# Kernel optimization log

Hardware: AMD Instinct MI355X
Metric: run time of the kernel (lower is better)

The kernel has to match this reference:

```python
import jax, jax.numpy as jnp
from jax import lax
import numpy as np

STRIDES = [4, 8, 16, 32, 64]
SIZES = [32, 64, 128, 256, 512]
RATIOS = [0.5, 1.0, 2.0]
PRE_NMS = 1000   # test-mode pre_nms_topk per level
POST_NMS = 1000  # test-mode post_nms_topk
NMS_THRESH = 0.7
NEG = -1e9
SCALE_CLAMP = float(np.log(1000.0 / 16.0))


def _anchor_bases(size):
    # one size, 3 aspect ratios (h/w); detectron2-style bases centered at 0
    area = float(size) * float(size)
    rows = []
    for ar in RATIOS:
        w = np.sqrt(area / ar)
        h = ar * w
        rows.append([-w / 2.0, -h / 2.0, w / 2.0, h / 2.0])
    return jnp.asarray(np.array(rows, dtype=np.float32))  # [3,4]


def _level_anchors(H, W, stride, bases):
    sx = jnp.arange(W, dtype=jnp.float32) * stride
    sy = jnp.arange(H, dtype=jnp.float32) * stride
    yy, xx = jnp.meshgrid(sy, sx, indexing='ij')
    shifts = jnp.stack([xx, yy, xx, yy], axis=-1).reshape(-1, 1, 4)  # [H*W,1,4]
    return (shifts + bases[None, :, :]).reshape(-1, 4)  # [H*W*3,4]


def _conv(x, w, b, pad):
    y = lax.conv_general_dilated(x, w, (1, 1), [(pad, pad), (pad, pad)],
                                 dimension_numbers=('NCHW', 'OIHW', 'NCHW'))
    return y + b[None, :, None, None]


def _decode(anchors, deltas):
    # anchors [R,4], deltas [B,R,4] -> boxes [B,R,4] (x1,y1,x2,y2)
    w = anchors[:, 2] - anchors[:, 0]
    h = anchors[:, 3] - anchors[:, 1]
    cx = anchors[:, 0] + 0.5 * w
    cy = anchors[:, 1] + 0.5 * h
    dx, dy = deltas[..., 0], deltas[..., 1]
    dw = jnp.minimum(deltas[..., 2], SCALE_CLAMP)
    dh = jnp.minimum(deltas[..., 3], SCALE_CLAMP)
    px = dx * w + cx
    py = dy * h + cy
    pw = jnp.exp(dw) * w
    ph = jnp.exp(dh) * h
    return jnp.stack([px - 0.5 * pw, py - 0.5 * ph, px + 0.5 * pw, py + 0.5 * ph], axis=-1)


def _pairwise_iou(b):
    x1 = jnp.maximum(b[:, None, 0], b[None, :, 0])
    y1 = jnp.maximum(b[:, None, 1], b[None, :, 1])
    x2 = jnp.minimum(b[:, None, 2], b[None, :, 2])
    y2 = jnp.minimum(b[:, None, 3], b[None, :, 3])
    inter = jnp.clip(x2 - x1, 0.0) * jnp.clip(y2 - y1, 0.0)
    area = (b[:, 2] - b[:, 0]) * (b[:, 3] - b[:, 1])
    return inter / (area[:, None] + area[None, :] - inter + 1e-9)


def _nms_single(boxes, scores, valid, lvls, img):
    # greedy batched NMS: level offsets keep levels from suppressing each other
    order = jnp.argsort(-scores)
    b = boxes[order]
    s = scores[order]
    v = valid[order]
    lv = lvls[order].astype(boxes.dtype)
    bo = b + lv[:, None] * (img + 1.0)
    iou = lax.stop_gradient(_pairwise_iou(bo))  # selection is non-differentiable
    T = b.shape[0]
    idxs = jnp.arange(T)

    def step(keep, i):
        supp = (iou[i] > NMS_THRESH) & (idxs > i) & keep[i]
        return keep & ~supp, None

    keep, _ = lax.scan(step, v, jnp.arange(T))
    final = jnp.where(keep, s, NEG)
    topv, topi = lax.top_k(final, POST_NMS)
    return b[topi], topv


def _rpn_forward(feats, w_inter, b_inter, w_logits, b_logits, w_reg, b_reg, image_size):
    img = float(image_size)
    cand_boxes, cand_scores, lvl_ids = [], [], []
    for l, (x, stride, size) in enumerate(zip(feats, STRIDES, SIZES)):
        B, _, H, W = x.shape
        inter = jax.nn.relu(_conv(x, w_inter, b_inter, 1))
        logit = _conv(inter, w_logits, b_logits, 0)        # [B,3,H,W]
        reg = _conv(inter, w_reg, b_reg, 0)                # [B,12,H,W]
        scores = logit.transpose(0, 2, 3, 1).reshape(B, -1)              # [B,H*W*3]
        deltas = reg.reshape(B, 3, 4, H, W).transpose(0, 3, 4, 1, 2).reshape(B, -1, 4)
        anchors = _level_anchors(H, W, stride, _anchor_bases(size))
        boxes = _decode(anchors, deltas)                                  # [B,R,4]
        k = min(PRE_NMS, scores.shape[1])
        topv, topi = lax.top_k(scores, k)
        cand_boxes.append(jnp.take_along_axis(boxes, topi[..., None], axis=1))
        cand_scores.append(topv)
        lvl_ids.append(jnp.full((k,), l, dtype=jnp.int32))
    boxes = jnp.concatenate(cand_boxes, axis=1)   # [B,T,4]
    scores = jnp.concatenate(cand_scores, axis=1) # [B,T]
    lvls = jnp.concatenate(lvl_ids, axis=0)       # [T]
    boxes = jnp.clip(boxes, 0.0, img)
    valid = (boxes[..., 2] > boxes[..., 0]) & (boxes[..., 3] > boxes[..., 1])
    kb, ks = jax.vmap(lambda b, s, v: _nms_single(b, s, v, lvls, img))(boxes, scores, valid)
    return jnp.concatenate([kb, ks[..., None]], axis=-1)  # [B,POST_NMS,5]


def setup_inputs() -> dict:
    key = jax.random.key(0)
    ks = jax.random.split(key, 16)
    C = 256
    inp = {
        'feat_p2': jax.random.normal(ks[0], (2, C, 256, 256), jnp.float32),
        'feat_p3': jax.random.normal(ks[1], (2, C, 128, 128), jnp.float32),
        'feat_p4': jax.random.normal(ks[2], (2, C, 64, 64), jnp.float32),
        'feat_p5': jax.random.normal(ks[3], (2, C, 32, 32), jnp.float32),
        'feat_p6': jax.random.normal(ks[4], (2, C, 16, 16), jnp.float32),
        'w_inter': jax.random.normal(ks[5], (C, C, 3, 3), jnp.float32) * 0.01,
        'b_inter': jnp.zeros((C,), jnp.float32),
        'w_logits': jax.random.normal(ks[6], (3, C, 1, 1), jnp.float32) * 0.01,
        'b_logits': jnp.zeros((3,), jnp.float32),
        'w_reg': jax.random.normal(ks[7], (12, C, 1, 1), jnp.float32) * 0.01,
        'b_reg': jnp.zeros((12,), jnp.float32),
        'image_size': 1024,
    }
    return inp


def reference(feat_p2, feat_p3, feat_p4, feat_p5, feat_p6,
              w_inter, b_inter, w_logits, b_logits, w_reg, b_reg, image_size):
    feats = [feat_p2, feat_p3, feat_p4, feat_p5, feat_p6]
    return _rpn_forward(feats, w_inter, b_inter, w_logits, b_logits, w_reg, b_reg, image_size)
```

## Files before the change

kernel.cpp:

```cpp
#include <hip/hip_runtime.h>
#include <cmath>

typedef unsigned int u32;
typedef unsigned long long u64;

#define TCAND 4768
#define RTOT  261888
#define NW    75
#define NROWS 4800
#define NEGV  -1e9f

__device__ __forceinline__ u32 fkey(float s){
  u32 u = __float_as_uint(s);
  return u ^ ((u >> 31) ? 0xFFFFFFFFu : 0x80000000u);
}

__device__ __forceinline__ void gload_lds16(const float* g, float* l){
  __builtin_amdgcn_global_load_lds((const __attribute__((address_space(1))) void*)g,
                                   (__attribute__((address_space(3))) void*)l, 16, 0, 0);
}
__device__ __forceinline__ void gload_lds4(const float* g, float* l){
  __builtin_amdgcn_global_load_lds((const __attribute__((address_space(1))) void*)g,
                                   (__attribute__((address_space(3))) void*)l, 4, 0, 0);
}

__device__ void bitonic_desc(u64* a, int N, int t, int nt){
  for (int len = 2; len <= N; len <<= 1){
    for (int inc = len >> 1; inc > 0; inc >>= 1){
      __syncthreads();
      for (int idx = t; idx < (N >> 1); idx += nt){
        int i = 2*idx - (idx & (inc - 1));
        int j = i + inc;
        u64 x = a[i], y = a[j];
        bool descR = ((i & len) == 0);
        bool sw = descR ? (x < y) : (x > y);
        if (sw){ a[i] = y; a[j] = x; }
      }
    }
  }
  __syncthreads();
}

__global__ void wtrans(const float* __restrict__ w, float* __restrict__ w_r2,
                       float* __restrict__ zbuf){
  if (blockIdx.x == 0 && threadIdx.x < 16) zbuf[threadIdx.x] = 0.f;
  int idx = blockIdx.x * 256 + threadIdx.x;
  if (idx >= 589824) return;
  int oc = idx / 2304;
  int r  = idx - oc * 2304;
  int ic = r / 9;
  int tap = r - ic * 9;
  w_r2[ic * 2304 + tap * 256 + oc] = w[idx];
}

template<int H, int STRIDEV, int ASIZE, int FOFF>
__device__ __forceinline__ void conv_level(
    int rel, const float* __restrict__ feat, const float* __restrict__ w_r2,
    const float* __restrict__ zbuf,
    const float* __restrict__ b_inter, const float* __restrict__ w_logits,
    const float* __restrict__ b_logits, const float* __restrict__ w_reg,
    const float* __restrict__ b_reg, const int* __restrict__ imgp,
    float* __restrict__ score_base, float* __restrict__ box_base,
    float* lds_w, float* lds_x, float* sbuf)
{
  constexpr int W = H;
  constexpr int TX = H / 8;
  constexpr int TILES = TX * TX;
  const int t = threadIdx.x;
  const int img = rel / TILES;
  const int tile = rel - img * TILES;
  const int x0 = (tile % TX) << 3;
  const int y0 = (tile / TX) << 3;
  const int lane = t & 63;
  const int ocg = lane;
  const int r = t >> 6;
  const int q = r;

  const size_t fb = (size_t)img * 256 * H * W;
  const size_t plane = (size_t)H * W;

  const float* xsrc = zbuf;
  size_t xstep = 0;
  if (q == 1 || q == 2){
    int cell = (q - 1) * 64 + lane;
    int xr = cell / 12, xc = cell - xr * 12;
    int gy = y0 + xr - 1, gx = x0 + xc - 1;
    bool ok = (cell < 120) && (xc < 10) && gy >= 0 && gy < H && gx >= 0 && gx < W;
    if (ok){ xsrc = feat + fb + (size_t)gy * W + gx; xstep = plane; }
  }

  const int c0 = 2 * q, c1 = 2 * q + 1;
  const int cex = (q == 0) ? 16 : ((q == 3) ? 17 : -1);

  float acc[32];
  #pragma unroll
  for (int j = 0; j < 32; j++) acc[j] = 0.f;

  #define STAGE(g_, sb) do { \
    const float* wg_ = w_r2 + (size_t)(g_) * 4608; \
    float* wl_ = lds_w + (sb) * 4608; \
    gload_lds16(wg_ + c0 * 256 + lane * 4, wl_ + c0 * 256); \
    gload_lds16(wg_ + c1 * 256 + lane * 4, wl_ + c1 * 256); \
    if (cex >= 0) gload_lds16(wg_ + cex * 256 + lane * 4, wl_ + cex * 256); \
    if (q == 1 || q == 2){ \
      gload_lds4(xsrc + (size_t)(2 * (g_)) * xstep, \
                 lds_x + (sb) * 256 + (q - 1) * 64); \
      gload_lds4(xsrc + (size_t)(2 * (g_) + 1) * xstep, \
                 lds_x + (sb) * 256 + 128 + (q - 1) * 64); \
    } \
  } while (0)

  STAGE(0, 0);

  int cur = 0;
  #pragma unroll 1
  for (int g = 0; g < 128; ++g){
    __builtin_amdgcn_s_barrier();
    __builtin_amdgcn_sched_barrier(0);
    if (g < 127){
      STAGE(g + 1, cur ^ 1);
    }
    __builtin_amdgcn_sched_barrier(0);
    if (g < 127){
      if (q == 1 || q == 2)      asm volatile("s_waitcnt vmcnt(4)" ::: "memory");
      else if (q == 0 || q == 3) asm volatile("s_waitcnt vmcnt(3)" ::: "memory");
      else                       asm volatile("s_waitcnt vmcnt(2)" ::: "memory");
    } else {
      asm volatile("s_waitcnt vmcnt(0)" ::: "memory");
    }
    __builtin_amdgcn_sched_barrier(0);
    __builtin_amdgcn_s_barrier();
    __builtin_amdgcn_sched_barrier(0);

    __builtin_amdgcn_s_setprio(1);
    const float* wbuf = lds_w + cur * 4608;
    const float* xbuf = lds_x + cur * 256;
    #pragma unroll 1
    for (int icl = 0; icl < 2; icl++){
      const float* wsub = wbuf + icl * 2304;
      const float* xsub = xbuf + icl * 128;
      #pragma unroll
      for (int ky = 0; ky < 3; ky++){
        float xrow[10];
        {
          const float* xp = xsub + (r + ky) * 12;
          *(float4*)&xrow[0] = *(const float4*)xp;
          *(float4*)&xrow[4] = *(const float4*)(xp + 4);
          *(float2*)&xrow[8] = *(const float2*)(xp + 8);
        }
        #pragma unroll
        for (int kx = 0; kx < 3; kx++){
          const int tap = ky * 3 + kx;
          float wk[4];
          *(float4*)&wk[0] = *(const float4*)(wsub + tap * 256 + ocg * 4);
          #pragma unroll
          for (int k = 0; k < 4; k++){
            #pragma unroll
            for (int c = 0; c < 8; c++)
              acc[k * 8 + c] = __builtin_fmaf(wk[k], xrow[c + kx], acc[k * 8 + c]);
          }
        }
      }
    }
    __builtin_amdgcn_s_setprio(0);
    cur ^= 1;
  }
  #undef STAGE

  {
    float bb[4];
    *(float4*)&bb[0] = *(const float4*)(b_inter + ocg * 4);
    #pragma unroll
    for (int k = 0; k < 4; k++)
      #pragma unroll
      for (int c = 0; c < 8; c++)
        acc[k * 8 + c] = fmaxf(acc[k * 8 + c] + bb[k], 0.f);
  }

  const int grp = ocg & 60;
  #pragma unroll 1
  for (int o = 0; o < 15; o++){
    const float* whp = (o < 3) ? (w_logits + o * 256) : (w_reg + (o - 3) * 256);
    float wh4[4];
    *(float4*)&wh4[0] = *(const float4*)(whp + ocg * 4);
    float fin[8];
    #pragma unroll
    for (int c = 0; c < 8; c++){
      float t1 = 0.f;
      #pragma unroll
      for (int k = 0; k < 4; k++) t1 = __builtin_fmaf(wh4[k], acc[k * 8 + c], t1);
      float b1 = __shfl(t1, grp);
      float t2 = b1;
      #pragma unroll
      for (int k = 0; k < 4; k++) t2 = __builtin_fmaf(wh4[k], acc[k * 8 + c], t2);
      float b2 = __shfl(t2, grp + 1);
      float t3 = b2;
      #pragma unroll
      for (int k = 0; k < 4; k++) t3 = __builtin_fmaf(wh4[k], acc[k * 8 + c], t3);
      float b3 = __shfl(t3, grp + 2);
      float t4 = b3;
      #pragma unroll
      for (int k = 0; k < 4; k++) t4 = __builtin_fmaf(wh4[k], acc[k * 8 + c], t4);
      float v = t4 + __shfl_xor(t4, 4);
      v = v + __shfl_xor(v, 8);
      v = v + __shfl_xor(v, 16);
      v = v + __shfl_xor(v, 32);
      fin[c] = v;
    }
    if (ocg == 3){
      #pragma unroll
      for (int c = 0; c < 8; c++) sbuf[(r * 8 + c) * 16 + o] = fin[c];
    }
  }
  __syncthreads();

  if (t < 192){
    int a = t >> 6; int px = t & 63;
    int rr = px >> 3, cc = px & 7;
    int y = y0 + rr, x = x0 + cc;
    float img_f = (float)(*imgp);
    float sc = sbuf[px * 16 + a] + b_logits[a];
    float d0 = sbuf[px * 16 + 3 + a * 4 + 0] + b_reg[a * 4 + 0];
    float d1 = sbuf[px * 16 + 3 + a * 4 + 1] + b_reg[a * 4 + 1];
    float d2 = sbuf[px * 16 + 3 + a * 4 + 2] + b_reg[a * 4 + 2];
    float d3 = sbuf[px * 16 + 3 + a * 4 + 3] + b_reg[a * 4 + 3];
    double ar = (a == 0) ? 0.5 : ((a == 1) ? 1.0 : 2.0);
    double area_d = (double)ASIZE * (double)ASIZE;
    double wd = sqrt(area_d / ar);
    double hd = ar * wd;
    float bx1 = (float)(-wd * 0.5), by1 = (float)(-hd * 0.5);
    float bx2 = (float)( wd * 0.5), by2 = (float)( hd * 0.5);
    float sx = (float)(x * STRIDEV), sy = (float)(y * STRIDEV);
    float ax1 = sx + bx1, ay1 = sy + by1, ax2 = sx + bx2, ay2 = sy + by2;
    float aw = __fsub_rn(ax2, ax1), ah = __fsub_rn(ay2, ay1);
    float acx = __fadd_rn(ax1, __fmul_rn(0.5f, aw));
    float acy = __fadd_rn(ay1, __fmul_rn(0.5f, ah));
    const float CLAMP = (float)4.135166556742356;
    float dwv = fminf(d2, CLAMP), dhv = fminf(d3, CLAMP);
    float pcx = __fadd_rn(__fmul_rn(d0, aw), acx);
    float pcy = __fadd_rn(__fmul_rn(d1, ah), acy);
    float pw = __fmul_rn((float)exp((double)dwv), aw);
    float ph = __fmul_rn((float)exp((double)dhv), ah);
    float hx = __fmul_rn(0.5f, pw), hy = __fmul_rn(0.5f, ph);
    float X1 = __fsub_rn(pcx, hx), Y1 = __fsub_rn(pcy, hy);
    float X2 = __fadd_rn(pcx, hx), Y2 = __fadd_rn(pcy, hy);
    X1 = fminf(fmaxf(X1, 0.f), img_f); Y1 = fminf(fmaxf(Y1, 0.f), img_f);
    X2 = fminf(fmaxf(X2, 0.f), img_f); Y2 = fminf(fmaxf(Y2, 0.f), img_f);
    int gi = (y * W + x) * 3 + a;
    size_t oidx = (size_t)img * RTOT + FOFF + gi;
    score_base[oidx] = sc;
    ((float4*)box_base)[oidx] = make_float4(X1, Y1, X2, Y2);
  }
}

__global__ __launch_bounds__(512, 4) void conv_all(
    const float* __restrict__ f2, const float* __restrict__ f3,
    const float* __restrict__ f4, const float* __restrict__ f5,
    const float* __restrict__ f6, const float* __restrict__ w_r2,
    const float* __restrict__ zbuf,
    const float* __restrict__ b_inter, const float* __restrict__ w_logits,
    const float* __restrict__ b_logits, const float* __restrict__ w_reg,
    const float* __restrict__ b_reg, const int* __restrict__ imgp,
    float* __restrict__ score_base, float* __restrict__ box_base)
{
  __shared__ float lds_w[2 * 4608];
  __shared__ float lds_x[2 * 256];
  float* sbuf = lds_w;
  const int bid = blockIdx.x;
  if (bid < 2048)
    conv_level<256, 4, 32, 0>(bid, f2, w_r2, zbuf, b_inter, w_logits, b_logits, w_reg,
                              b_reg, imgp, score_base, box_base, lds_w, lds_x, sbuf);
  else if (bid < 2560)
    conv_level<128, 8, 64, 196608>(bid - 2048, f3, w_r2, zbuf, b_inter, w_logits, b_logits,
                                   w_reg, b_reg, imgp, score_base, box_base, lds_w, lds_x, sbuf);
  else if (bid < 2688)
    conv_level<64, 16, 128, 245760>(bid - 2560, f4, w_r2, zbuf, b_inter, w_logits, b_logits,
                                    w_reg, b_reg, imgp, score_base, box_base, lds_w, lds_x, sbuf);
  else if (bid < 2720)
    conv_level<32, 32, 256, 258048>(bid - 2688, f5, w_r2, zbuf, b_inter, w_logits, b_logits,
                                    w_reg, b_reg, imgp, score_base, box_base, lds_w, lds_x, sbuf);
  else
    conv_level<16, 64, 512, 261120>(bid - 2720, f6, w_r2, zbuf, b_inter, w_logits, b_logits,
                                    w_reg, b_reg, imgp, score_base, box_base, lds_w, lds_x, sbuf);
}

__global__ __launch_bounds__(1024) void topk_lvl(
    const float* __restrict__ score_base, const float* __restrict__ box_base,
    float* __restrict__ cs, float* __restrict__ cb, int* __restrict__ clvl)
{
  const int lvl = blockIdx.x, b = blockIdx.y;
  const int Rtab[5] = {196608, 49152, 12288, 3072, 768};
  const int Ktab[5] = {1000, 1000, 1000, 1000, 768};
  const int Ftab[5] = {0, 196608, 245760, 258048, 261120};
  const int Ctab[5] = {0, 1000, 2000, 3000, 4000};
  const int R = Rtab[lvl], kk = Ktab[lvl], foff = Ftab[lvl], coff = Ctab[lvl];
  const float* sc = score_base + (size_t)b * RTOT + foff;
  const int t = threadIdx.x;
  const int wv = t >> 6;
  __shared__ u32 histp[16 * 256];
  __shared__ u32 hist[256];
  __shared__ u32 sh_prefix, sh_r;
  __shared__ u32 cgt, ceq;
  __shared__ u64 sel[1024];
  __shared__ u64 eqb[1024];
  if (t == 0){ sh_prefix = 0u; sh_r = (u32)kk; }
  __syncthreads();
  for (int pass = 0; pass < 4; ++pass){
    for (int i = t; i < 4096; i += 1024) histp[i] = 0u;
    __syncthreads();
    u32 prefix = sh_prefix;
    int shift = 24 - 8 * pass;
    u32 maskHi = (pass == 0) ? 0u : (0xFFFFFFFFu << (shift + 8));
    for (int i = t; i < R; i += 1024){
      u32 key = fkey(sc[i]);
      if ((key & maskHi) == prefix) atomicAdd(&histp[wv * 256 + ((key >> shift) & 255u)], 1u);
    }
    __syncthreads();
    if (t < 256){
      u32 s = 0;
      #pragma unroll
      for (int w2 = 0; w2 < 16; w2++) s += histp[w2 * 256 + t];
      hist[t] = s;
    }
    __syncthreads();
    if (t == 0){
      u32 r = sh_r; u32 run = 0; int chosen = 255;
      for (int bv = 255; bv >= 0; --bv){
        u32 c = hist[bv];
        if (run + c >= r){ chosen = bv; break; }
        run += c;
      }
      sh_prefix = prefix | ((u32)chosen << shift);
      sh_r = r - run;
    }
    __syncthreads();
  }
  const u32 Tkey = sh_prefix; const u32 need_eq = sh_r;
  if (t == 0){ cgt = 0u; ceq = 0u; }
  __syncthreads();
  for (int i = t; i < R; i += 1024){
    u32 key = fkey(sc[i]);
    if (key > Tkey){
      u32 p = atomicAdd(&cgt, 1u);
      sel[p] = (((u64)key) << 32) | (u64)(0xFFFFFFFFu - (u32)i);
    } else if (key == Tkey){
      u32 e = atomicAdd(&ceq, 1u);
      if (e < 1024u) eqb[e] = (u64)(0xFFFFFFFFu - (u32)i);
    }
  }
  __syncthreads();
  u32 nGt = cgt; u32 nEq = ceq > 1024u ? 1024u : ceq;
  if ((u32)t >= nEq) eqb[t] = 0ull;
  __syncthreads();
  bitonic_desc(eqb, 1024, t, 1024);
  if ((u32)t < need_eq) sel[nGt + t] = (((u64)Tkey) << 32) | (eqb[t] & 0xFFFFFFFFull);
  if (t >= kk) sel[t] = 0ull;
  __syncthreads();
  bitonic_desc(sel, 1024, t, 1024);
  if (t < kk){
    u64 v = sel[t];
    u32 i = 0xFFFFFFFFu - (u32)(v & 0xFFFFFFFFull);
    int dst = b * TCAND + coff + t;
    cs[dst] = sc[i];
    ((float4*)cb)[dst] = ((const float4*)box_base)[(size_t)b * RTOT + foff + i];
    clvl[dst] = lvl;
  }
}

__global__ __launch_bounds__(1024) void gsort(
    const float* __restrict__ cs, const float* __restrict__ cb, const int* __restrict__ clvl,
    const int* __restrict__ imgp,
    float* __restrict__ s_score, float* __restrict__ s_box, float* __restrict__ obox,
    float* __restrict__ area, int* __restrict__ validarr)
{
  const int b = blockIdx.x, t = threadIdx.x;
  __shared__ u64 arr[8192];
  for (int i = t; i < 8192; i += 1024){
    u64 v = 0ull;
    if (i < TCAND){
      u32 key = fkey(cs[b * TCAND + i]);
      v = (((u64)key) << 32) | (u64)(0xFFFFFFFFu - (u32)i);
    }
    arr[i] = v;
  }
  __syncthreads();
  bitonic_desc(arr, 8192, t, 1024);
  const float img = (float)(*imgp);
  const float off1 = img + 1.0f;
  for (int s = t; s < TCAND; s += 1024){
    u32 ci = 0xFFFFFFFFu - (u32)(arr[s] & 0xFFFFFFFFull);
    int src = b * TCAND + (int)ci;
    int dst = b * TCAND + s;
    float scv = cs[src];
    float4 bx = ((const float4*)cb)[src];
    s_score[dst] = scv;
    ((float4*)s_box)[dst] = bx;
    float lv = (float)clvl[src];
    float tt = __fmul_rn(lv, off1);
    float o0 = __fadd_rn(bx.x, tt), o1 = __fadd_rn(bx.y, tt);
    float o2 = __fadd_rn(bx.z, tt), o3 = __fadd_rn(bx.w, tt);
    ((float4*)obox)[dst] = make_float4(o0, o1, o2, o3);
    area[dst] = __fmul_rn(__fsub_rn(o2, o0), __fsub_rn(o3, o1));
    validarr[dst] = (bx.z > bx.x && bx.w > bx.y) ? 1 : 0;
  }
}

__global__ void iou_mat(const float* __restrict__ obox, const float* __restrict__ area,
                        u64* __restrict__ supp)
{
  const int b = blockIdx.y;
  int wid = blockIdx.x * 256 + threadIdx.x;
  const int total = NW * TCAND;
  if (wid >= total) return;
  int w = wid / TCAND;
  int i = wid - w * TCAND;
  float4 bi = ((const float4*)obox)[b * TCAND + i];
  float ai = area[b * TCAND + i];
  u64 bits = 0ull;
  int jbase = w << 6;
  for (int jj = 0; jj < 64; jj++){
    int j = jbase + jj;
    if (j >= TCAND) break;
    if (j <= i) continue;
    float4 bj = ((const float4*)obox)[b * TCAND + j];
    float xx1 = fmaxf(bi.x, bj.x), yy1 = fmaxf(bi.y, bj.y);
    float xx2 = fminf(bi.z, bj.z), yy2 = fminf(bi.w, bj.w);
    float iw = fmaxf(__fsub_rn(xx2, xx1), 0.f);
    float ih = fmaxf(__fsub_rn(yy2, yy1), 0.f);
    float inter = __fmul_rn(iw, ih);
    float uni = __fadd_rn(__fsub_rn(__fadd_rn(ai, area[b * TCAND + j]), inter), 1e-9f);
    float iou = inter / uni;
    if (iou > 0.7f) bits |= (1ull << jj);
  }
  supp[((size_t)b * NROWS + i) * NW + w] = bits;
}

__global__ __launch_bounds__(64) void nms_scan(const u64* __restrict__ supp,
                                               const int* __restrict__ validarr,
                                               u64* __restrict__ keep_out)
{
  const int b = blockIdx.x;
  const int lane = threadIdx.x;
  u64 rlo = 0ull, rhi = 0ull;
  for (int jj = 0; jj < 64; jj++){
    int i1 = (lane << 6) + jj;
    u64 bad1 = (i1 < TCAND) ? (validarr[b * TCAND + i1] ? 0ull : 1ull) : 1ull;
    rlo |= bad1 << jj;
    int i2 = ((lane + 64) << 6) + jj;
    u64 bad2 = (i2 < TCAND) ? (validarr[b * TCAND + i2] ? 0ull : 1ull) : 1ull;
    rhi |= bad2 << jj;
  }
  for (int c = 0; c < NW; c++){
    u64 rw = (c < 64) ? __shfl(rlo, c) : __shfl(rhi, c - 64);
    u64 diag = supp[((size_t)b * NROWS + (c << 6) + lane) * NW + c];
    for (int s = 0; s < 64; s++){
      if (!((rw >> s) & 1ull)) rw |= __shfl(diag, s);
    }
    if (c < 64){ if (lane == c) rlo = rw; }
    else       { if (lane == c - 64) rhi = rw; }
    u64 kept = ~rw;
    const u64* rowbase = supp + ((size_t)b * NROWS + (c << 6)) * NW;
    u64 rem = kept;
    while (rem){
      int s0 = (int)__builtin_ctzll(rem); rem &= rem - 1;
      int s1 = s0, s2 = s0, s3 = s0;
      if (rem){ s1 = (int)__builtin_ctzll(rem); rem &= rem - 1; }
      if (rem){ s2 = (int)__builtin_ctzll(rem); rem &= rem - 1; }
      if (rem){ s3 = (int)__builtin_ctzll(rem); rem &= rem - 1; }
      u64 a0 = rowbase[(size_t)s0 * NW + lane];
      u64 a1 = rowbase[(size_t)s1 * NW + lane];
      u64 a2 = rowbase[(size_t)s2 * NW + lane];
      u64 a3 = rowbase[(size_t)s3 * NW + lane];
      rlo |= (a0 | a1) | (a2 | a3);
      if (lane < 11){
        u64 h0 = rowbase[(size_t)s0 * NW + 64 + lane];
        u64 h1 = rowbase[(size_t)s1 * NW + 64 + lane];
        u64 h2 = rowbase[(size_t)s2 * NW + 64 + lane];
        u64 h3 = rowbase[(size_t)s3 * NW + 64 + lane];
        rhi |= (h0 | h1) | (h2 | h3);
      }
    }
  }
  keep_out[b * 80 + lane] = ~rlo;
  if (lane < 11) keep_out[b * 80 + 64 + lane] = ~rhi;
}

__global__ __launch_bounds__(1024) void emit(const u64* __restrict__ keep_out,
                                             const float* __restrict__ s_score,
                                             const float* __restrict__ s_box,
                                             float* __restrict__ out)
{
  const int b = blockIdx.x, t = threadIdx.x;
  __shared__ int part[1024];
  int f[5]; int base = t * 5; int lsum = 0;
  #pragma unroll
  for (int q = 0; q < 5; q++){
    int s = base + q; int kp = 0;
    if (s < TCAND) kp = (int)((keep_out[b * 80 + (s >> 6)] >> (s & 63)) & 1ull);
    f[q] = kp; lsum += kp;
  }
  part[t] = lsum;
  __syncthreads();
  for (int d = 1; d < 1024; d <<= 1){
    int addv = 0;
    if (t >= d) addv = part[t - d];
    __syncthreads();
    part[t] += addv;
    __syncthreads();
  }
  int K = part[1023];
  int kcnt = part[t] - lsum;
  #pragma unroll
  for (int q = 0; q < 5; q++){
    int s = base + q;
    if (s < TCAND){
      int pos = f[q] ? kcnt : (K + (s - kcnt));
      if (pos < 1000){
        float4 bx = ((const float4*)s_box)[b * TCAND + s];
        float scv = f[q] ? s_score[b * TCAND + s] : NEGV;
        float* o = out + ((size_t)b * 1000 + pos) * 5;
        o[0] = bx.x; o[1] = bx.y; o[2] = bx.z; o[3] = bx.w; o[4] = scv;
      }
      kcnt += f[q];
    }
  }
}

extern "C" void kernel_launch(void* const* d_in, const int* in_sizes, int n_in,
                              void* d_out, int out_size, void* d_ws, size_t ws_size,
                              hipStream_t stream)
{
  (void)in_sizes; (void)n_in; (void)out_size; (void)ws_size;
  const float* f2 = (const float*)d_in[0];
  const float* f3 = (const float*)d_in[1];
  const float* f4 = (const float*)d_in[2];
  const float* f5 = (const float*)d_in[3];
  const float* f6 = (const float*)d_in[4];
  const float* w_inter  = (const float*)d_in[5];
  const float* b_inter  = (const float*)d_in[6];
  const float* w_logits = (const float*)d_in[7];
  const float* b_logits = (const float*)d_in[8];
  const float* w_reg    = (const float*)d_in[9];
  const float* b_reg    = (const float*)d_in[10];
  const int*   imgp     = (const int*)d_in[11];

  char* ws = (char*)d_ws;
  float* w_r2       = (float*)(ws + 0);
  float* score_base = (float*)(ws + 2359296);
  float* box_base   = (float*)(ws + 4454400);
  float* cs         = (float*)(ws + 12834816);
  float* cb         = (float*)(ws + 12872960);
  int*   clvl       = (int*)  (ws + 13025536);
  float* s_score    = (float*)(ws + 13063680);
  float* s_box      = (float*)(ws + 13101824);
  float* obox       = (float*)(ws + 13254400);
  float* area       = (float*)(ws + 13406976);
  int*   validarr   = (int*)  (ws + 13445120);
  u64*   supp       = (u64*)  (ws + 13483264);
  u64*   keep_out   = (u64*)  (ws + 19243264);
  float* zbuf       = (float*)(ws + 13483264);

  hipLaunchKernelGGL(wtrans, dim3((589824 + 255) / 256), dim3(256), 0, stream,
                     w_inter, w_r2, zbuf);

  hipLaunchKernelGGL(conv_all, dim3(2728), dim3(512), 0, stream,
                     f2, f3, f4, f5, f6, w_r2, zbuf, b_inter, w_logits, b_logits,
                     w_reg, b_reg, imgp, score_base, box_base);

  hipLaunchKernelGGL(topk_lvl, dim3(5, 2), dim3(1024), 0, stream,
                     score_base, box_base, cs, cb, clvl);
  hipLaunchKernelGGL(gsort, dim3(2), dim3(1024), 0, stream,
                     cs, cb, clvl, imgp, s_score, s_box, obox, area, validarr);
  hipLaunchKernelGGL(iou_mat, dim3((NW * TCAND + 255) / 256, 2), dim3(256), 0, stream,
                     obox, area, supp);
  hipLaunchKernelGGL(nms_scan, dim3(2), dim3(64), 0, stream, supp, validarr, keep_out);
  hipLaunchKernelGGL(emit, dim3(2), dim3(1024), 0, stream, keep_out, s_score, s_box,
                     (float*)d_out);
}
```

Baseline: 3.880 ms.

## Remap conv wave tiling to two output rows by half the channels

Each wave now computes two output rows for half the 256 output channels (two channels per lane), where before it computed one row for all channels (four per lane). Input rows loaded from LDS are reused across adjacent output rows, so each icl step reads 4 rows instead of 3 per ky, and each weight load is a float2 instead of a float4. The head reduction becomes a shuffle chain over 8 lanes, and each channel half writes partial sums to a separate sbuf region, which the epilogue adds together. This trades LDS read traffic for a longer shuffle reduction and twice the sbuf footprint.

```diff
diff --git a/kernel.cpp b/kernel.cpp
--- a/kernel.cpp
+++ b/kernel.cpp
@@ -73,8 +73,10 @@
   const int y0 = (tile / TX) << 3;
   const int lane = t & 63;
   const int ocg = lane;
-  const int r = t >> 6;
-  const int q = r;
+  const int wv = t >> 6;
+  const int h = wv & 1;
+  const int p = wv >> 1;
+  const int q = wv;
 
   const size_t fb = (size_t)img * 256 * H * W;
   const size_t plane = (size_t)H * W;
@@ -110,6 +112,20 @@
     } \
   } while (0)
 
+  #define KYTAP(XA, XB, KY) do { \
+    _Pragma("unroll") \
+    for (int kx = 0; kx < 3; kx++){ \
+      const float2 wk = *(const float2*)(wsub + ((KY) * 3 + kx) * 256); \
+      _Pragma("unroll") \
+      for (int c = 0; c < 8; c++){ \
+        acc[c]      = __builtin_fmaf(wk.x, (XA)[c + kx], acc[c]); \
+        acc[8 + c]  = __builtin_fmaf(wk.x, (XB)[c + kx], acc[8 + c]); \
+        acc[16 + c] = __builtin_fmaf(wk.y, (XA)[c + kx], acc[16 + c]); \
+        acc[24 + c] = __builtin_fmaf(wk.y, (XB)[c + kx], acc[24 + c]); \
+      } \
+    } \
+  } while (0)
+
   STAGE(0, 0);
 
   int cur = 0;
@@ -137,79 +153,58 @@
     const float* xbuf = lds_x + cur * 256;
     #pragma unroll 1
     for (int icl = 0; icl < 2; icl++){
-      const float* wsub = wbuf + icl * 2304;
+      const float* wsub = wbuf + icl * 2304 + h * 128 + (ocg << 1);
       const float* xsub = xbuf + icl * 128;
-      #pragma unroll
-      for (int ky = 0; ky < 3; ky++){
-        float xrow[10];
-        {
-          const float* xp = xsub + (r + ky) * 12;
-          *(float4*)&xrow[0] = *(const float4*)xp;
-          *(float4*)&xrow[4] = *(const float4*)(xp + 4);
-          *(float2*)&xrow[8] = *(const float2*)(xp + 8);
-        }
-        #pragma unroll
-        for (int kx = 0; kx < 3; kx++){
-          const int tap = ky * 3 + kx;
-          float wk[4];
-          *(float4*)&wk[0] = *(const float4*)(wsub + tap * 256 + ocg * 4);
-          #pragma unroll
-          for (int k = 0; k < 4; k++){
-            #pragma unroll
-            for (int c = 0; c < 8; c++)
-              acc[k * 8 + c] = __builtin_fmaf(wk[k], xrow[c + kx], acc[k * 8 + c]);
-          }
-        }
+      float R0[10], R1[10], R2[10], R3[10];
+      {
+        const float* rp = xsub + (2 * p) * 12;
+        *(float4*)&R0[0] = *(const float4*)rp;       *(float4*)&R0[4] = *(const float4*)(rp + 4);
+        *(float2*)&R0[8] = *(const float2*)(rp + 8);
+        *(float4*)&R1[0] = *(const float4*)(rp + 12); *(float4*)&R1[4] = *(const float4*)(rp + 16);
+        *(float2*)&R1[8] = *(const float2*)(rp + 20);
+        *(float4*)&R2[0] = *(const float4*)(rp + 24); *(float4*)&R2[4] = *(const float4*)(rp + 28);
+        *(float2*)&R2[8] = *(const float2*)(rp + 32);
+        *(float4*)&R3[0] = *(const float4*)(rp + 36); *(float4*)&R3[4] = *(const float4*)(rp + 40);
+        *(float2*)&R3[8] = *(const float2*)(rp + 44);
       }
+      KYTAP(R0, R1, 0);
+      KYTAP(R1, R2, 1);
+      KYTAP(R2, R3, 2);
     }
     __builtin_amdgcn_s_setprio(0);
     cur ^= 1;
   }
   #undef STAGE
+  #undef KYTAP
 
   {
-    float bb[4];
-    *(float4*)&bb[0] = *(const float4*)(b_inter + ocg * 4);
+    const float2 bb = *(const float2*)(b_inter + h * 128 + (ocg << 1));
     #pragma unroll
-    for (int k = 0; k < 4; k++)
-      #pragma unroll
-      for (int c = 0; c < 8; c++)
-        acc[k * 8 + c] = fmaxf(acc[k * 8 + c] + bb[k], 0.f);
-  }
-
-  const int grp = ocg & 60;
+    for (int c = 0; c < 16; c++){
+      acc[c]      = fmaxf(acc[c] + bb.x, 0.f);
+      acc[16 + c] = fmaxf(acc[16 + c] + bb.y, 0.f);
+    }
+  }
+
+  const int grp = ocg & 56;
   #pragma unroll 1
   for (int o = 0; o < 15; o++){
     const float* whp = (o < 3) ? (w_logits + o * 256) : (w_reg + (o - 3) * 256);
-    float wh4[4];
-    *(float4*)&wh4[0] = *(const float4*)(whp + ocg * 4);
-    float fin[8];
+    const float2 wh = *(const float2*)(whp + h * 128 + (ocg << 1));
     #pragma unroll
-    for (int c = 0; c < 8; c++){
-      float t1 = 0.f;
+    for (int c = 0; c < 16; c++){
+      float tv = __builtin_fmaf(wh.x, acc[c], 0.f);
+      tv = __builtin_fmaf(wh.y, acc[16 + c], tv);
       #pragma unroll
-      for (int k = 0; k < 4; k++) t1 = __builtin_fmaf(wh4[k], acc[k * 8 + c], t1);
-      float b1 = __shfl(t1, grp);
-      float t2 = b1;
-      #pragma unroll
-      for (int k = 0; k < 4; k++) t2 = __builtin_fmaf(wh4[k], acc[k * 8 + c], t2);
-      float b2 = __shfl(t2, grp + 1);
-      float t3 = b2;
-      #pragma unroll
-      for (int k = 0; k < 4; k++) t3 = __builtin_fmaf(wh4[k], acc[k * 8 + c], t3);
-      float b3 = __shfl(t3, grp + 2);
-      float t4 = b3;
-      #pragma unroll
-      for (int k = 0; k < 4; k++) t4 = __builtin_fmaf(wh4[k], acc[k * 8 + c], t4);
-      float v = t4 + __shfl_xor(t4, 4);
-      v = v + __shfl_xor(v, 8);
+      for (int s = 0; s < 7; s++){
+        float bb = __shfl(tv, grp + s);
+        float t2 = __builtin_fmaf(wh.x, acc[c], bb);
+        tv = __builtin_fmaf(wh.y, acc[16 + c], t2);
+      }
+      float v = tv + __shfl_xor(tv, 8);
       v = v + __shfl_xor(v, 16);
       v = v + __shfl_xor(v, 32);
-      fin[c] = v;
-    }
-    if (ocg == 3){
-      #pragma unroll
-      for (int c = 0; c < 8; c++) sbuf[(r * 8 + c) * 16 + o] = fin[c];
+      if (ocg == 7) sbuf[h * 1024 + (p * 16 + c) * 16 + o] = v;
     }
   }
   __syncthreads();
@@ -219,11 +214,13 @@
     int rr = px >> 3, cc = px & 7;
     int y = y0 + rr, x = x0 + cc;
     float img_f = (float)(*imgp);
-    float sc = sbuf[px * 16 + a] + b_logits[a];
-    float d0 = sbuf[px * 16 + 3 + a * 4 + 0] + b_reg[a * 4 + 0];
-    float d1 = sbuf[px * 16 + 3 + a * 4 + 1] + b_reg[a * 4 + 1];
-    float d2 = sbuf[px * 16 + 3 + a * 4 + 2] + b_reg[a * 4 + 2];
-    float d3 = sbuf[px * 16 + 3 + a * 4 + 3] + b_reg[a * 4 + 3];
+    #define FIN(o) (sbuf[(px * 16) + (o)] + sbuf[1024 + (px * 16) + (o)])
+    float sc = FIN(a) + b_logits[a];
+    float d0 = FIN(3 + a * 4 + 0) + b_reg[a * 4 + 0];
+    float d1 = FIN(3 + a * 4 + 1) + b_reg[a * 4 + 1];
+    float d2 = FIN(3 + a * 4 + 2) + b_reg[a * 4 + 2];
+    float d3 = FIN(3 + a * 4 + 3) + b_reg[a * 4 + 3];
+    #undef FIN
     double ar = (a == 0) ? 0.5 : ((a == 1) ? 1.0 : 2.0);
     double area_d = (double)ASIZE * (double)ASIZE;
     double wd = sqrt(area_d / ar);
```

Result: slower. 4.313 ms (+11.2%).
